# Performance work log

Hardware: AMD Instinct MI355X
Metric: run time of the kernel (lower is better)

The kernel has to match this reference:

```python
import jax, jax.numpy as jnp
import numpy as np


def _lin(x, w, b):
    # torch Linear: y = x @ w.T + b, w shape [out, in]
    return x @ w.T + b


def setup_inputs() -> dict:
    key = jax.random.key(0)
    ks = jax.random.split(key, 24)
    D, L1, L2, L3, C = 784, 128, 64, 32, 10
    B = 65536
    s = 0.05
    inp = {
        'x': jax.random.normal(ks[0], (B, D), jnp.float32),
        'W1_w': jax.random.normal(ks[1], (L1, D), jnp.float32) * s,
        'W1_b': jnp.zeros((L1,), jnp.float32),
        'U1_w': jax.random.normal(ks[2], (L1, L1), jnp.float32) * s,
        'U1_b': jnp.zeros((L1,), jnp.float32),
        'W2_w': jax.random.normal(ks[3], (L2, L1), jnp.float32) * s,
        'W2_b': jnp.zeros((L2,), jnp.float32),
        'U2_w': jax.random.normal(ks[4], (L2, L2), jnp.float32) * s,
        'U2_b': jnp.zeros((L2,), jnp.float32),
        'W3_w': jax.random.normal(ks[5], (L3, L2), jnp.float32) * s,
        'W3_b': jnp.zeros((L3,), jnp.float32),
        'U3_w': jax.random.normal(ks[6], (L3, L3), jnp.float32) * s,
        'U3_b': jnp.zeros((L3,), jnp.float32),
        'fb3_w': jax.random.normal(ks[7], (L2, L3), jnp.float32) * s,
        'fb3_b': jnp.zeros((L2,), jnp.float32),
        'fb2_w': jax.random.normal(ks[8], (L1, L2), jnp.float32) * s,
        'fb2_b': jnp.zeros((L1,), jnp.float32),
        'fb1_w': jax.random.normal(ks[9], (D, L1), jnp.float32) * s,
        'fb1_b': jnp.zeros((D,), jnp.float32),
        'clf_w': jax.random.normal(ks[10], (C, L3), jnp.float32) * s,
        'clf_b': jnp.zeros((C,), jnp.float32),
        'steps': 5,
    }
    return inp


def reference(x, W1_w, W1_b, U1_w, U1_b, W2_w, W2_b, U2_w, U2_b,
              W3_w, W3_b, U3_w, U3_b, fb3_w, fb3_b, fb2_w, fb2_b,
              fb1_w, fb1_b, clf_w, clf_b, steps):
    B = x.shape[0]
    x = x.reshape(B, -1)
    h1 = jnp.zeros((B, W1_w.shape[0]), x.dtype)
    h2 = jnp.zeros((B, W2_w.shape[0]), x.dtype)
    h3 = jnp.zeros((B, W3_w.shape[0]), x.dtype)
    for _ in range(steps):  # fixed small step count (5)
        err_h2 = h2 - _lin(h3, fb3_w, fb3_b)
        err_h1 = h1 - _lin(h2, fb2_w, fb2_b)
        err_x = x - _lin(h1, fb1_w, fb1_b)
        h3 = h3 + jnp.tanh(_lin(err_h2, W3_w, W3_b)) + jnp.tanh(_lin(h3, U3_w, U3_b))
        h2 = h2 + jnp.tanh(_lin(err_h1, W2_w, W2_b)) + jnp.tanh(_lin(h2, U2_w, U2_b))
        h1 = h1 + jnp.tanh(_lin(err_x, W1_w, W1_b)) + jnp.tanh(_lin(h1, U1_w, U1_b))
    return _lin(h3, clf_w, clf_b)
```

## Files before the change

kernel.cpp:

```cpp
#include <hip/hip_runtime.h>
#include <stdint.h>

typedef __attribute__((ext_vector_type(8))) __bf16 bf16x8;
typedef __attribute__((ext_vector_type(8))) unsigned short u16x8;
typedef __attribute__((ext_vector_type(4))) float f32x4;

#define WSF_M1 0
#define WSF_M2 16384
#define WSF_M3 20480
#define WSF_C  21504
#define F_W1T 0
#define F_M1N 102400
#define F_U1T 118784
#define F_W2T 135168
#define F_M2N 143360
#define F_U2T 147456
#define F_W3T 151552
#define F_M3N 153600
#define F_U3T 154624
#define F_CLF 155648

__device__ __forceinline__ unsigned short f2bf(float f) {
  uint32_t u = __builtin_bit_cast(uint32_t, f);
  u += 0x7fffu + ((u >> 16) & 1u);
  return (unsigned short)(u >> 16);
}

extern "C" __device__ float __ocml_native_exp2_f32(float);
__device__ __forceinline__ float tanh_fast(float x) {
  float e = __ocml_native_exp2_f32(x * 2.8853900817779268f);
  return 1.0f - 2.0f * __builtin_amdgcn_rcpf(e + 1.0f);
}

__device__ __forceinline__ f32x4 mfma16(bf16x8 a, bf16x8 b, f32x4 c) {
  return __builtin_amdgcn_mfma_f32_16x16x32_bf16(a, b, c, 0, 0, 0);
}

__device__ __forceinline__ bf16x8 lds_frag(const unsigned short* p) {
  u16x8 v = *(const u16x8*)p;
  return __builtin_bit_cast(bf16x8, v);
}
__device__ __forceinline__ bf16x8 glb_frag(const unsigned short* __restrict__ base,
                                           int fi, int lane) {
  u16x8 v = *(const u16x8*)(base + (((size_t)fi * 64 + lane) << 3));
  return __builtin_bit_cast(bf16x8, v);
}

__global__ void pcnet_prep(
    const float* __restrict__ W1_w, const float* __restrict__ W1_b,
    const float* __restrict__ W2_w, const float* __restrict__ W2_b,
    const float* __restrict__ W3_w, const float* __restrict__ W3_b,
    const float* __restrict__ fb1_w, const float* __restrict__ fb1_b,
    const float* __restrict__ fb2_w, const float* __restrict__ fb2_b,
    const float* __restrict__ fb3_w, const float* __restrict__ fb3_b,
    float* __restrict__ wsf)
{
  const int b = threadIdx.x;
  const int blk = blockIdx.x;
  if (blk < 128) {
    const int a = blk;
    float s = 0.f;
    for (int d = 0; d < 784; ++d) s += fb1_w[d*128 + a] * W1_w[b*784 + d];
    wsf[WSF_M1 + a*128 + b] = -s;
  } else if (blk < 192) {
    const int a = blk - 128;
    if (b < 64) {
      float s = 0.f;
      for (int d = 0; d < 128; ++d) s += fb2_w[d*64 + a] * W2_w[b*128 + d];
      wsf[WSF_M2 + a*64 + b] = -s;
    }
  } else if (blk < 224) {
    const int a = blk - 192;
    if (b < 32) {
      float s = 0.f;
      for (int d = 0; d < 64; ++d) s += fb3_w[d*32 + a] * W3_w[b*64 + d];
      wsf[WSF_M3 + a*32 + b] = -s;
    }
  } else if (blk == 224) {
    float s = 0.f;
    for (int d = 0; d < 784; ++d) s += fb1_b[d] * W1_w[b*784 + d];
    wsf[WSF_C + b] = W1_b[b] - s;
  } else if (blk == 225) {
    if (b < 64) {
      float s = 0.f;
      for (int d = 0; d < 128; ++d) s += fb2_b[d] * W2_w[b*128 + d];
      wsf[WSF_C + 128 + b] = W2_b[b] - s;
    }
  } else {
    if (b < 32) {
      float s = 0.f;
      for (int d = 0; d < 64; ++d) s += fb3_b[d] * W3_w[b*64 + d];
      wsf[WSF_C + 192 + b] = W3_b[b] - s;
    }
  }
}

__device__ __forceinline__ void swz_T(const float* __restrict__ src, int ld, int Kv, int Nv,
                                      int NT, unsigned short* __restrict__ dst, int f, int lane) {
  const int kt = f / NT, nt = f - kt*NT;
  const int m = lane & 15, q = lane >> 4;
  const int n = nt*16 + m;
  u16x8 v;
#pragma unroll
  for (int j = 0; j < 8; ++j) {
    const int k = kt*32 + q*8 + j;
    float val = (k < Kv && n < Nv) ? src[(size_t)n*ld + k] : 0.f;
    v[j] = f2bf(val);
  }
  *(u16x8*)(dst + (((size_t)f*64 + lane) << 3)) = v;
}
__device__ __forceinline__ void swz_R(const float* __restrict__ src, int N, int NT,
                                      unsigned short* __restrict__ dst, int f, int lane) {
  const int kt = f / NT, nt = f - kt*NT;
  const int m = lane & 15, q = lane >> 4;
  const int n = nt*16 + m;
  u16x8 v;
#pragma unroll
  for (int j = 0; j < 8; ++j) {
    const int k = kt*32 + q*8 + j;
    v[j] = f2bf(src[k*N + n]);
  }
  *(u16x8*)(dst + (((size_t)f*64 + lane) << 3)) = v;
}

__global__ void pcnet_swz(
    const float* __restrict__ W1_w, const float* __restrict__ U1_w,
    const float* __restrict__ W2_w, const float* __restrict__ U2_w,
    const float* __restrict__ W3_w, const float* __restrict__ U3_w,
    const float* __restrict__ clf_w, const float* __restrict__ wsf,
    unsigned short* __restrict__ frags)
{
  const int t = blockIdx.x*256 + threadIdx.x;
  if (t >= 305*64) return;
  const int fg = t >> 6, lane = t & 63;
  if      (fg < 200) swz_T(W1_w, 784, 784, 128, 8, frags + F_W1T, fg,       lane);
  else if (fg < 232) swz_R(wsf + WSF_M1, 128, 8,  frags + F_M1N, fg - 200, lane);
  else if (fg < 264) swz_T(U1_w, 128, 128, 128, 8, frags + F_U1T, fg - 232, lane);
  else if (fg < 280) swz_T(W2_w, 128, 128, 64, 4, frags + F_W2T, fg - 264, lane);
  else if (fg < 288) swz_R(wsf + WSF_M2, 64, 4,   frags + F_M2N, fg - 280, lane);
  else if (fg < 296) swz_T(U2_w, 64, 64, 64, 4,   frags + F_U2T, fg - 288, lane);
  else if (fg < 300) swz_T(W3_w, 64, 64, 32, 2,   frags + F_W3T, fg - 296, lane);
  else if (fg < 302) swz_R(wsf + WSF_M3, 32, 2,   frags + F_M3N, fg - 300, lane);
  else if (fg < 304) swz_T(U3_w, 32, 32, 32, 2,   frags + F_U3T, fg - 302, lane);
  else               swz_T(clf_w, 32, 32, 10, 1,  frags + F_CLF, fg - 304, lane);
}

__global__ __launch_bounds__(256, 2)
void pcnet_main(
    const float* __restrict__ x,
    const float* __restrict__ cvec,
    const float* __restrict__ U1_b, const float* __restrict__ U2_b,
    const float* __restrict__ U3_b, const float* __restrict__ clf_b,
    const unsigned short* __restrict__ frags,
    const int* __restrict__ steps_p,
    float* __restrict__ out)
{
  const int tid  = threadIdx.x;
  const int wave = tid >> 6;
  const int lane = tid & 63;
  const int q = lane >> 4;
  const int m = lane & 15;
  const int rowBase = blockIdx.x << 6;

  __shared__ unsigned short h1b[64*136];
  __shared__ unsigned short h2b[64*72];
  __shared__ unsigned short h3b[64*40];
  __shared__ unsigned short xst[2][64*40];

  const unsigned short* fW1T = frags + F_W1T;
  const unsigned short* fM1N = frags + F_M1N;
  const unsigned short* fU1T = frags + F_U1T;
  const unsigned short* fW2T = frags + F_W2T;
  const unsigned short* fM2N = frags + F_M2N;
  const unsigned short* fU2T = frags + F_U2T;
  const unsigned short* fW3T = frags + F_W3T;
  const unsigned short* fM3N = frags + F_M3N;
  const unsigned short* fU3T = frags + F_U3T;
  const unsigned short* fCLF = frags + F_CLF;

  f32x4 A1[4][2];
#pragma unroll
  for (int nt = 0; nt < 2; ++nt) {
    const float cv = cvec[(2*wave + nt)*16 + m];
    const f32x4 v = {cv, cv, cv, cv};
    A1[0][nt] = v; A1[1][nt] = v; A1[2][nt] = v; A1[3][nt] = v;
  }

  const int srow = tid >> 2;
  const int kq = (tid & 3) << 3;
  const float* __restrict__ xrow = x + (size_t)(rowBase + srow)*784;

  {
    f32x4 va = *(const f32x4*)(xrow + kq);
    f32x4 vb = *(const f32x4*)(xrow + kq + 4);
    u16x8 pk;
    pk[0]=f2bf(va[0]); pk[1]=f2bf(va[1]); pk[2]=f2bf(va[2]); pk[3]=f2bf(va[3]);
    pk[4]=f2bf(vb[0]); pk[5]=f2bf(vb[1]); pk[6]=f2bf(vb[2]); pk[7]=f2bf(vb[3]);
    *(u16x8*)(xst[0] + srow*40 + kq) = pk;
  }

  for (int kt = 0; kt < 25; ++kt) {
    __syncthreads();
    if (kt < 24) {
      const int gk = (kt + 1)*32 + kq;
      f32x4 va = {0.f,0.f,0.f,0.f}, vb = {0.f,0.f,0.f,0.f};
      if (gk < 784) { va = *(const f32x4*)(xrow + gk); vb = *(const f32x4*)(xrow + gk + 4); }
      u16x8 pk;
      pk[0]=f2bf(va[0]); pk[1]=f2bf(va[1]); pk[2]=f2bf(va[2]); pk[3]=f2bf(va[3]);
      pk[4]=f2bf(vb[0]); pk[5]=f2bf(vb[1]); pk[6]=f2bf(vb[2]); pk[7]=f2bf(vb[3]);
      *(u16x8*)(xst[(kt+1)&1] + srow*40 + kq) = pk;
    }
    const unsigned short* xb = xst[kt & 1];
    const bf16x8 a0 = lds_frag(xb + (0*16 + m)*40 + q*8);
    const bf16x8 a1 = lds_frag(xb + (1*16 + m)*40 + q*8);
    const bf16x8 a2 = lds_frag(xb + (2*16 + m)*40 + q*8);
    const bf16x8 a3 = lds_frag(xb + (3*16 + m)*40 + q*8);
#pragma unroll
    for (int nt = 0; nt < 2; ++nt) {
      const bf16x8 b = glb_frag(fW1T, kt*8 + 2*wave + nt, lane);
      A1[0][nt] = mfma16(a0, b, A1[0][nt]);
      A1[1][nt] = mfma16(a1, b, A1[1][nt]);
      A1[2][nt] = mfma16(a2, b, A1[2][nt]);
      A1[3][nt] = mfma16(a3, b, A1[3][nt]);
    }
  }

  {
    uint32_t* p = (uint32_t*)h1b;
    for (int i = tid; i < 4352; i += 256) p[i] = 0u;
    p = (uint32_t*)h2b;
    for (int i = tid; i < 2304; i += 256) p[i] = 0u;
    p = (uint32_t*)h3b;
    for (int i = tid; i < 1280; i += 256) p[i] = 0u;
  }
  f32x4 h1v[4][2], h2v[4], h3v[2];
  {
    const f32x4 z = {0.f,0.f,0.f,0.f};
#pragma unroll
    for (int rt = 0; rt < 4; ++rt) { h1v[rt][0] = z; h1v[rt][1] = z; h2v[rt] = z; }
    h3v[0] = z; h3v[1] = z;
  }

  const int nt3 = wave >> 1;
  const int rt3 = (wave & 1) << 1;
  const float c3v  = cvec[192 + nt3*16 + m];
  const float b3v  = U3_b[nt3*16 + m];
  const float c2v  = cvec[128 + wave*16 + m];
  const float b2v  = U2_b[wave*16 + m];
  const float b1v0 = U1_b[(2*wave + 0)*16 + m];
  const float b1v1 = U1_b[(2*wave + 1)*16 + m];

  __syncthreads();

  const int S = *steps_p;
  for (int s = 0; s < S; ++s) {
    bf16x8 h2f[2][4];
#pragma unroll
    for (int kt = 0; kt < 2; ++kt)
#pragma unroll
      for (int rt = 0; rt < 4; ++rt)
        h2f[kt][rt] = lds_frag(h2b + (rt*16 + m)*72 + kt*32 + q*8);
    const bf16x8 h3f0 = lds_frag(h3b + ((rt3+0)*16 + m)*40 + q*8);
    const bf16x8 h3f1 = lds_frag(h3b + ((rt3+1)*16 + m)*40 + q*8);
    bf16x8 h2s0[2], h2s1[2];
#pragma unroll
    for (int kt = 0; kt < 2; ++kt) {
      h2s0[kt] = (wave & 1) ? h2f[kt][2] : h2f[kt][0];
      h2s1[kt] = (wave & 1) ? h2f[kt][3] : h2f[kt][1];
    }

    f32x4 z3a0 = {c3v,c3v,c3v,c3v}, z3a1 = z3a0;
    f32x4 z3b0 = {b3v,b3v,b3v,b3v}, z3b1 = z3b0;
#pragma unroll
    for (int kt = 0; kt < 2; ++kt) {
      const bf16x8 b = glb_frag(fW3T, kt*2 + nt3, lane);
      z3a0 = mfma16(h2s0[kt], b, z3a0);
      z3a1 = mfma16(h2s1[kt], b, z3a1);
    }
    { const bf16x8 b = glb_frag(fM3N, nt3, lane);
      z3a0 = mfma16(h3f0, b, z3a0); z3a1 = mfma16(h3f1, b, z3a1); }
    { const bf16x8 b = glb_frag(fU3T, nt3, lane);
      z3b0 = mfma16(h3f0, b, z3b0); z3b1 = mfma16(h3f1, b, z3b1); }
#pragma unroll
    for (int r = 0; r < 4; ++r) {
      h3v[0][r] += tanh_fast(z3a0[r]) + tanh_fast(z3b0[r]);
      h3v[1][r] += tanh_fast(z3a1[r]) + tanh_fast(z3b1[r]);
    }

    f32x4 z2b[4];
    { const f32x4 v = {b2v,b2v,b2v,b2v}; z2b[0]=v; z2b[1]=v; z2b[2]=v; z2b[3]=v; }
#pragma unroll
    for (int kt = 0; kt < 2; ++kt) {
      const bf16x8 b = glb_frag(fU2T, kt*4 + wave, lane);
#pragma unroll
      for (int rt = 0; rt < 4; ++rt) z2b[rt] = mfma16(h2f[kt][rt], b, z2b[rt]);
    }
#pragma unroll
    for (int rt = 0; rt < 4; ++rt)
#pragma unroll
      for (int r = 0; r < 4; ++r) h2v[rt][r] += tanh_fast(z2b[rt][r]);

    f32x4 z2a[4];
    { const f32x4 v = {c2v,c2v,c2v,c2v}; z2a[0]=v; z2a[1]=v; z2a[2]=v; z2a[3]=v; }
#pragma unroll
    for (int kt = 0; kt < 2; ++kt) {
      const bf16x8 b = glb_frag(fM2N, kt*4 + wave, lane);
#pragma unroll
      for (int rt = 0; rt < 4; ++rt) z2a[rt] = mfma16(h2f[kt][rt], b, z2a[rt]);
    }

    f32x4 z1a[4][2], z1b[4][2];
    { const f32x4 v0 = {b1v0,b1v0,b1v0,b1v0};
      const f32x4 v1 = {b1v1,b1v1,b1v1,b1v1};
#pragma unroll
      for (int rt = 0; rt < 4; ++rt) {
        z1a[rt][0] = A1[rt][0]; z1a[rt][1] = A1[rt][1];
        z1b[rt][0] = v0;        z1b[rt][1] = v1;
      }
    }
#pragma unroll
    for (int kt = 0; kt < 4; ++kt) {
      const bf16x8 a0 = lds_frag(h1b + (0*16 + m)*136 + kt*32 + q*8);
      const bf16x8 a1 = lds_frag(h1b + (1*16 + m)*136 + kt*32 + q*8);
      const bf16x8 a2 = lds_frag(h1b + (2*16 + m)*136 + kt*32 + q*8);
      const bf16x8 a3 = lds_frag(h1b + (3*16 + m)*136 + kt*32 + q*8);
      const bf16x8 bW = glb_frag(fW2T, kt*4 + wave, lane);
      z2a[0] = mfma16(a0, bW, z2a[0]);
      z2a[1] = mfma16(a1, bW, z2a[1]);
      z2a[2] = mfma16(a2, bW, z2a[2]);
      z2a[3] = mfma16(a3, bW, z2a[3]);
      const bf16x8 bM0 = glb_frag(fM1N, kt*8 + 2*wave + 0, lane);
      const bf16x8 bM1 = glb_frag(fM1N, kt*8 + 2*wave + 1, lane);
      z1a[0][0] = mfma16(a0, bM0, z1a[0][0]); z1a[0][1] = mfma16(a0, bM1, z1a[0][1]);
      z1a[1][0] = mfma16(a1, bM0, z1a[1][0]); z1a[1][1] = mfma16(a1, bM1, z1a[1][1]);
      z1a[2][0] = mfma16(a2, bM0, z1a[2][0]); z1a[2][1] = mfma16(a2, bM1, z1a[2][1]);
      z1a[3][0] = mfma16(a3, bM0, z1a[3][0]); z1a[3][1] = mfma16(a3, bM1, z1a[3][1]);
      const bf16x8 bU0 = glb_frag(fU1T, kt*8 + 2*wave + 0, lane);
      const bf16x8 bU1 = glb_frag(fU1T, kt*8 + 2*wave + 1, lane);
      z1b[0][0] = mfma16(a0, bU0, z1b[0][0]); z1b[0][1] = mfma16(a0, bU1, z1b[0][1]);
      z1b[1][0] = mfma16(a1, bU0, z1b[1][0]); z1b[1][1] = mfma16(a1, bU1, z1b[1][1]);
      z1b[2][0] = mfma16(a2, bU0, z1b[2][0]); z1b[2][1] = mfma16(a2, bU1, z1b[2][1]);
      z1b[3][0] = mfma16(a3, bU0, z1b[3][0]); z1b[3][1] = mfma16(a3, bU1, z1b[3][1]);
    }
#pragma unroll
    for (int rt = 0; rt < 4; ++rt)
#pragma unroll
      for (int r = 0; r < 4; ++r) h2v[rt][r] += tanh_fast(z2a[rt][r]);
#pragma unroll
    for (int rt = 0; rt < 4; ++rt)
#pragma unroll
      for (int nt = 0; nt < 2; ++nt)
#pragma unroll
        for (int r = 0; r < 4; ++r)
          h1v[rt][nt][r] += tanh_fast(z1a[rt][nt][r]) + tanh_fast(z1b[rt][nt][r]);

    __syncthreads();
#pragma unroll
    for (int rt = 0; rt < 4; ++rt) {
#pragma unroll
      for (int nt = 0; nt < 2; ++nt)
#pragma unroll
        for (int r = 0; r < 4; ++r)
          h1b[(rt*16 + q*4 + r)*136 + (2*wave + nt)*16 + m] = f2bf(h1v[rt][nt][r]);
#pragma unroll
      for (int r = 0; r < 4; ++r)
        h2b[(rt*16 + q*4 + r)*72 + wave*16 + m] = f2bf(h2v[rt][r]);
    }
#pragma unroll
    for (int i = 0; i < 2; ++i)
#pragma unroll
      for (int r = 0; r < 4; ++r)
        h3b[((rt3 + i)*16 + q*4 + r)*40 + nt3*16 + m] = f2bf(h3v[i][r]);
    __syncthreads();
  }

  f32x4 o;
  { const float cb = (m < 10) ? clf_b[m] : 0.f; o = (f32x4){cb, cb, cb, cb}; }
  {
    const bf16x8 a = lds_frag(h3b + (wave*16 + m)*40 + q*8);
    const bf16x8 b = glb_frag(fCLF, 0, lane);
    o = mfma16(a, b, o);
  }
  if (m < 10) {
#pragma unroll
    for (int r = 0; r < 4; ++r) {
      const int row = rowBase + wave*16 + q*4 + r;
      out[(size_t)row*10 + m] = o[r];
    }
  }
}

extern "C" void kernel_launch(void* const* d_in, const int* in_sizes, int n_in,
                              void* d_out, int out_size, void* d_ws, size_t ws_size,
                              hipStream_t stream)
{
  (void)in_sizes; (void)n_in; (void)out_size; (void)ws_size;
  const float* x     = (const float*)d_in[0];
  const float* W1_w  = (const float*)d_in[1];
  const float* W1_b  = (const float*)d_in[2];
  const float* U1_w  = (const float*)d_in[3];
  const float* U1_b  = (const float*)d_in[4];
  const float* W2_w  = (const float*)d_in[5];
  const float* W2_b  = (const float*)d_in[6];
  const float* U2_w  = (const float*)d_in[7];
  const float* U2_b  = (const float*)d_in[8];
  const float* W3_w  = (const float*)d_in[9];
  const float* W3_b  = (const float*)d_in[10];
  const float* U3_w  = (const float*)d_in[11];
  const float* U3_b  = (const float*)d_in[12];
  const float* fb3_w = (const float*)d_in[13];
  const float* fb3_b = (const float*)d_in[14];
  const float* fb2_w = (const float*)d_in[15];
  const float* fb2_b = (const float*)d_in[16];
  const float* fb1_w = (const float*)d_in[17];
  const float* fb1_b = (const float*)d_in[18];
  const float* clf_w = (const float*)d_in[19];
  const float* clf_b = (const float*)d_in[20];
  const int*   steps = (const int*)d_in[21];

  float* wsf = (float*)d_ws;
  unsigned short* frags = (unsigned short*)d_ws + 43520;

  hipLaunchKernelGGL(pcnet_prep, dim3(227), dim3(128), 0, stream,
                     W1_w, W1_b, W2_w, W2_b, W3_w, W3_b,
                     fb1_w, fb1_b, fb2_w, fb2_b, fb3_w, fb3_b, wsf);
  hipLaunchKernelGGL(pcnet_swz, dim3(77), dim3(256), 0, stream,
                     W1_w, U1_w, W2_w, U2_w, W3_w, U3_w, clf_w, wsf, frags);
  hipLaunchKernelGGL(pcnet_main, dim3(1024), dim3(256), 0, stream,
                     x, wsf + WSF_C, U1_b, U2_b, U3_b, clf_b, frags, steps,
                     (float*)d_out);
}
```

Baseline: 545.6 us.

## Halve main-kernel row tile to 32 and parallelize prep dot products per wave

The prep kernel is rewritten so each 64-lane wave computes one output dot product with strided loads and a shuffle reduction, instead of one thread looping serially over up to 784 elements. This targets the long serial latency of the old 227-block launch. The main kernel processes 32 rows per block instead of 64, which doubles the grid to 2048 blocks and halves per-block LDS and accumulator registers to allow more occupancy. The cost is that each block re-reads the swizzled weight fragments for half as many rows, and the final classifier uses only two of the four waves.

After: 480.5 us. -11.9%, faster.

```diff
diff --git a/kernel.cpp b/kernel.cpp
--- a/kernel.cpp
+++ b/kernel.cpp
@@ -3,6 +3,7 @@
 
 typedef __attribute__((ext_vector_type(8))) __bf16 bf16x8;
 typedef __attribute__((ext_vector_type(8))) unsigned short u16x8;
+typedef __attribute__((ext_vector_type(4))) unsigned short u16x4;
 typedef __attribute__((ext_vector_type(4))) float f32x4;
 
 #define WSF_M1 0
@@ -46,7 +47,8 @@
   return __builtin_bit_cast(bf16x8, v);
 }
 
-__global__ void pcnet_prep(
+__global__ __launch_bounds__(256)
+void pcnet_prep(
     const float* __restrict__ W1_w, const float* __restrict__ W1_b,
     const float* __restrict__ W2_w, const float* __restrict__ W2_b,
     const float* __restrict__ W3_w, const float* __restrict__ W3_b,
@@ -55,43 +57,37 @@
     const float* __restrict__ fb3_w, const float* __restrict__ fb3_b,
     float* __restrict__ wsf)
 {
-  const int b = threadIdx.x;
-  const int blk = blockIdx.x;
-  if (blk < 128) {
-    const int a = blk;
-    float s = 0.f;
-    for (int d = 0; d < 784; ++d) s += fb1_w[d*128 + a] * W1_w[b*784 + d];
-    wsf[WSF_M1 + a*128 + b] = -s;
-  } else if (blk < 192) {
-    const int a = blk - 128;
-    if (b < 64) {
-      float s = 0.f;
-      for (int d = 0; d < 128; ++d) s += fb2_w[d*64 + a] * W2_w[b*128 + d];
-      wsf[WSF_M2 + a*64 + b] = -s;
-    }
-  } else if (blk < 224) {
-    const int a = blk - 192;
-    if (b < 32) {
-      float s = 0.f;
-      for (int d = 0; d < 64; ++d) s += fb3_w[d*32 + a] * W3_w[b*64 + d];
-      wsf[WSF_M3 + a*32 + b] = -s;
-    }
-  } else if (blk == 224) {
-    float s = 0.f;
-    for (int d = 0; d < 784; ++d) s += fb1_b[d] * W1_w[b*784 + d];
-    wsf[WSF_C + b] = W1_b[b] - s;
-  } else if (blk == 225) {
-    if (b < 64) {
-      float s = 0.f;
-      for (int d = 0; d < 128; ++d) s += fb2_b[d] * W2_w[b*128 + d];
-      wsf[WSF_C + 128 + b] = W2_b[b] - s;
-    }
-  } else {
-    if (b < 32) {
-      float s = 0.f;
-      for (int d = 0; d < 64; ++d) s += fb3_b[d] * W3_w[b*64 + d];
-      wsf[WSF_C + 192 + b] = W3_b[b] - s;
-    }
+  const int w    = blockIdx.x * 4 + (threadIdx.x >> 6);
+  const int lane = threadIdx.x & 63;
+  float s = 0.f;
+  if (w < 16384) {
+    const int a = w >> 7, b = w & 127;
+    for (int d = lane; d < 784; d += 64) s += fb1_w[d*128 + a] * W1_w[b*784 + d];
+  } else if (w < 20480) {
+    const int t = w - 16384, a = t >> 6, b = t & 63;
+    for (int d = lane; d < 128; d += 64) s += fb2_w[d*64 + a] * W2_w[b*128 + d];
+  } else if (w < 21504) {
+    const int t = w - 20480, a = t >> 5, b = t & 31;
+    s = fb3_w[lane*32 + a] * W3_w[b*64 + lane];
+  } else if (w < 21632) {
+    const int b = w - 21504;
+    for (int d = lane; d < 784; d += 64) s += fb1_b[d] * W1_w[b*784 + d];
+  } else if (w < 21696) {
+    const int b = w - 21632;
+    for (int d = lane; d < 128; d += 64) s += fb2_b[d] * W2_w[b*128 + d];
+  } else if (w < 21728) {
+    const int b = w - 21696;
+    s = fb3_b[lane] * W3_w[b*64 + lane];
+  }
+#pragma unroll
+  for (int off = 32; off >= 1; off >>= 1) s += __shfl_down(s, off, 64);
+  if (lane == 0) {
+    if (w < 16384)      wsf[WSF_M1 + (w >> 7)*128 + (w & 127)] = -s;
+    else if (w < 20480) { const int t = w - 16384; wsf[WSF_M2 + (t >> 6)*64 + (t & 63)] = -s; }
+    else if (w < 21504) { const int t = w - 20480; wsf[WSF_M3 + (t >> 5)*32 + (t & 31)] = -s; }
+    else if (w < 21632) { const int b = w - 21504; wsf[WSF_C + b]       = W1_b[b] - s; }
+    else if (w < 21696) { const int b = w - 21632; wsf[WSF_C + 128 + b] = W2_b[b] - s; }
+    else if (w < 21728) { const int b = w - 21696; wsf[WSF_C + 192 + b] = W3_b[b] - s; }
   }
 }
 
@@ -160,12 +156,12 @@
   const int lane = tid & 63;
   const int q = lane >> 4;
   const int m = lane & 15;
-  const int rowBase = blockIdx.x << 6;
-
-  __shared__ unsigned short h1b[64*136];
-  __shared__ unsigned short h2b[64*72];
-  __shared__ unsigned short h3b[64*40];
-  __shared__ unsigned short xst[2][64*40];
+  const int rowBase = blockIdx.x << 5;
+
+  __shared__ unsigned short h1b[32*136];
+  __shared__ unsigned short h2b[32*72];
+  __shared__ unsigned short h3b[32*40];
+  __shared__ unsigned short xst[2][32*40];
 
   const unsigned short* fW1T = frags + F_W1T;
   const unsigned short* fM1N = frags + F_M1N;
@@ -178,71 +174,64 @@
   const unsigned short* fU3T = frags + F_U3T;
   const unsigned short* fCLF = frags + F_CLF;
 
-  f32x4 A1[4][2];
+  f32x4 A1[2][2];
 #pragma unroll
   for (int nt = 0; nt < 2; ++nt) {
     const float cv = cvec[(2*wave + nt)*16 + m];
     const f32x4 v = {cv, cv, cv, cv};
-    A1[0][nt] = v; A1[1][nt] = v; A1[2][nt] = v; A1[3][nt] = v;
-  }
-
-  const int srow = tid >> 2;
-  const int kq = (tid & 3) << 3;
+    A1[0][nt] = v; A1[1][nt] = v;
+  }
+
+  const int srow = tid >> 3;
+  const int kq   = (tid & 7) << 2;
   const float* __restrict__ xrow = x + (size_t)(rowBase + srow)*784;
 
   {
     f32x4 va = *(const f32x4*)(xrow + kq);
-    f32x4 vb = *(const f32x4*)(xrow + kq + 4);
-    u16x8 pk;
+    u16x4 pk;
     pk[0]=f2bf(va[0]); pk[1]=f2bf(va[1]); pk[2]=f2bf(va[2]); pk[3]=f2bf(va[3]);
-    pk[4]=f2bf(vb[0]); pk[5]=f2bf(vb[1]); pk[6]=f2bf(vb[2]); pk[7]=f2bf(vb[3]);
-    *(u16x8*)(xst[0] + srow*40 + kq) = pk;
+    *(u16x4*)(xst[0] + srow*40 + kq) = pk;
   }
 
   for (int kt = 0; kt < 25; ++kt) {
     __syncthreads();
     if (kt < 24) {
       const int gk = (kt + 1)*32 + kq;
-      f32x4 va = {0.f,0.f,0.f,0.f}, vb = {0.f,0.f,0.f,0.f};
-      if (gk < 784) { va = *(const f32x4*)(xrow + gk); vb = *(const f32x4*)(xrow + gk + 4); }
-      u16x8 pk;
+      f32x4 va = {0.f,0.f,0.f,0.f};
+      if (gk < 784) va = *(const f32x4*)(xrow + gk);
+      u16x4 pk;
       pk[0]=f2bf(va[0]); pk[1]=f2bf(va[1]); pk[2]=f2bf(va[2]); pk[3]=f2bf(va[3]);
-      pk[4]=f2bf(vb[0]); pk[5]=f2bf(vb[1]); pk[6]=f2bf(vb[2]); pk[7]=f2bf(vb[3]);
-      *(u16x8*)(xst[(kt+1)&1] + srow*40 + kq) = pk;
+      *(u16x4*)(xst[(kt+1)&1] + srow*40 + kq) = pk;
     }
     const unsigned short* xb = xst[kt & 1];
     const bf16x8 a0 = lds_frag(xb + (0*16 + m)*40 + q*8);
     const bf16x8 a1 = lds_frag(xb + (1*16 + m)*40 + q*8);
-    const bf16x8 a2 = lds_frag(xb + (2*16 + m)*40 + q*8);
-    const bf16x8 a3 = lds_frag(xb + (3*16 + m)*40 + q*8);
 #pragma unroll
     for (int nt = 0; nt < 2; ++nt) {
       const bf16x8 b = glb_frag(fW1T, kt*8 + 2*wave + nt, lane);
       A1[0][nt] = mfma16(a0, b, A1[0][nt]);
       A1[1][nt] = mfma16(a1, b, A1[1][nt]);
-      A1[2][nt] = mfma16(a2, b, A1[2][nt]);
-      A1[3][nt] = mfma16(a3, b, A1[3][nt]);
     }
   }
 
   {
     uint32_t* p = (uint32_t*)h1b;
-    for (int i = tid; i < 4352; i += 256) p[i] = 0u;
+    for (int i = tid; i < 2176; i += 256) p[i] = 0u;
     p = (uint32_t*)h2b;
-    for (int i = tid; i < 2304; i += 256) p[i] = 0u;
+    for (int i = tid; i < 1152; i += 256) p[i] = 0u;
     p = (uint32_t*)h3b;
-    for (int i = tid; i < 1280; i += 256) p[i] = 0u;
-  }
-  f32x4 h1v[4][2], h2v[4], h3v[2];
+    for (int i = tid; i < 640; i += 256) p[i] = 0u;
+  }
+  f32x4 h1v[2][2], h2v[2], h3v;
   {
     const f32x4 z = {0.f,0.f,0.f,0.f};
 #pragma unroll
-    for (int rt = 0; rt < 4; ++rt) { h1v[rt][0] = z; h1v[rt][1] = z; h2v[rt] = z; }
-    h3v[0] = z; h3v[1] = z;
+    for (int rt = 0; rt < 2; ++rt) { h1v[rt][0] = z; h1v[rt][1] = z; h2v[rt] = z; }
+    h3v = z;
   }
 
   const int nt3 = wave >> 1;
-  const int rt3 = (wave & 1) << 1;
+  const int rt3 = wave & 1;
   const float c3v  = cvec[192 + nt3*16 + m];
   const float b3v  = U3_b[nt3*16 + m];
   const float c2v  = cvec[128 + wave*16 + m];
@@ -254,66 +243,57 @@
 
   const int S = *steps_p;
   for (int s = 0; s < S; ++s) {
-    bf16x8 h2f[2][4];
+    bf16x8 h2f[2][2];
 #pragma unroll
     for (int kt = 0; kt < 2; ++kt)
 #pragma unroll
-      for (int rt = 0; rt < 4; ++rt)
+      for (int rt = 0; rt < 2; ++rt)
         h2f[kt][rt] = lds_frag(h2b + (rt*16 + m)*72 + kt*32 + q*8);
-    const bf16x8 h3f0 = lds_frag(h3b + ((rt3+0)*16 + m)*40 + q*8);
-    const bf16x8 h3f1 = lds_frag(h3b + ((rt3+1)*16 + m)*40 + q*8);
-    bf16x8 h2s0[2], h2s1[2];
-#pragma unroll
-    for (int kt = 0; kt < 2; ++kt) {
-      h2s0[kt] = (wave & 1) ? h2f[kt][2] : h2f[kt][0];
-      h2s1[kt] = (wave & 1) ? h2f[kt][3] : h2f[kt][1];
-    }
-
-    f32x4 z3a0 = {c3v,c3v,c3v,c3v}, z3a1 = z3a0;
-    f32x4 z3b0 = {b3v,b3v,b3v,b3v}, z3b1 = z3b0;
+    const bf16x8 h3f = lds_frag(h3b + (rt3*16 + m)*40 + q*8);
+    bf16x8 h2s[2];
+#pragma unroll
+    for (int kt = 0; kt < 2; ++kt) h2s[kt] = (wave & 1) ? h2f[kt][1] : h2f[kt][0];
+
+    f32x4 z3a = {c3v,c3v,c3v,c3v};
+    f32x4 z3b = {b3v,b3v,b3v,b3v};
 #pragma unroll
     for (int kt = 0; kt < 2; ++kt) {
       const bf16x8 b = glb_frag(fW3T, kt*2 + nt3, lane);
-      z3a0 = mfma16(h2s0[kt], b, z3a0);
-      z3a1 = mfma16(h2s1[kt], b, z3a1);
-    }
-    { const bf16x8 b = glb_frag(fM3N, nt3, lane);
-      z3a0 = mfma16(h3f0, b, z3a0); z3a1 = mfma16(h3f1, b, z3a1); }
-    { const bf16x8 b = glb_frag(fU3T, nt3, lane);
-      z3b0 = mfma16(h3f0, b, z3b0); z3b1 = mfma16(h3f1, b, z3b1); }
-#pragma unroll
-    for (int r = 0; r < 4; ++r) {
-      h3v[0][r] += tanh_fast(z3a0[r]) + tanh_fast(z3b0[r]);
-      h3v[1][r] += tanh_fast(z3a1[r]) + tanh_fast(z3b1[r]);
-    }
-
-    f32x4 z2b[4];
-    { const f32x4 v = {b2v,b2v,b2v,b2v}; z2b[0]=v; z2b[1]=v; z2b[2]=v; z2b[3]=v; }
+      z3a = mfma16(h2s[kt], b, z3a);
+    }
+    { const bf16x8 b = glb_frag(fM3N, nt3, lane); z3a = mfma16(h3f, b, z3a); }
+    { const bf16x8 b = glb_frag(fU3T, nt3, lane); z3b = mfma16(h3f, b, z3b); }
+#pragma unroll
+    for (int r = 0; r < 4; ++r)
+      h3v[r] += tanh_fast(z3a[r]) + tanh_fast(z3b[r]);
+
+    f32x4 z2b[2];
+    { const f32x4 v = {b2v,b2v,b2v,b2v}; z2b[0]=v; z2b[1]=v; }
 #pragma unroll
     for (int kt = 0; kt < 2; ++kt) {
       const bf16x8 b = glb_frag(fU2T, kt*4 + wave, lane);
 #pragma unroll
-      for (int rt = 0; rt < 4; ++rt) z2b[rt] = mfma16(h2f[kt][rt], b, z2b[rt]);
-    }
-#pragma unroll
-    for (int rt = 0; rt < 4; ++rt)
+      for (int rt = 0; rt < 2; ++rt) z2b[rt] = mfma16(h2f[kt][rt], b, z2b[rt]);
+    }
+#pragma unroll
+    for (int rt = 0; rt < 2; ++rt)
 #pragma unroll
       for (int r = 0; r < 4; ++r) h2v[rt][r] += tanh_fast(z2b[rt][r]);
 
-    f32x4 z2a[4];
-    { const f32x4 v = {c2v,c2v,c2v,c2v}; z2a[0]=v; z2a[1]=v; z2a[2]=v; z2a[3]=v; }
+    f32x4 z2a[2];
+    { const f32x4 v = {c2v,c2v,c2v,c2v}; z2a[0]=v; z2a[1]=v; }
 #pragma unroll
     for (int kt = 0; kt < 2; ++kt) {
       const bf16x8 b = glb_frag(fM2N, kt*4 + wave, lane);
 #pragma unroll
-      for (int rt = 0; rt < 4; ++rt) z2a[rt] = mfma16(h2f[kt][rt], b, z2a[rt]);
-    }
-
-    f32x4 z1a[4][2], z1b[4][2];
+      for (int rt = 0; rt < 2; ++rt) z2a[rt] = mfma16(h2f[kt][rt], b, z2a[rt]);
+    }
+
+    f32x4 z1a[2][2], z1b[2][2];
     { const f32x4 v0 = {b1v0,b1v0,b1v0,b1v0};
       const f32x4 v1 = {b1v1,b1v1,b1v1,b1v1};
 #pragma unroll
-      for (int rt = 0; rt < 4; ++rt) {
+      for (int rt = 0; rt < 2; ++rt) {
         z1a[rt][0] = A1[rt][0]; z1a[rt][1] = A1[rt][1];
         z1b[rt][0] = v0;        z1b[rt][1] = v1;
       }
@@ -322,32 +302,24 @@
     for (int kt = 0; kt < 4; ++kt) {
       const bf16x8 a0 = lds_frag(h1b + (0*16 + m)*136 + kt*32 + q*8);
       const bf16x8 a1 = lds_frag(h1b + (1*16 + m)*136 + kt*32 + q*8);
-      const bf16x8 a2 = lds_frag(h1b + (2*16 + m)*136 + kt*32 + q*8);
-      const bf16x8 a3 = lds_frag(h1b + (3*16 + m)*136 + kt*32 + q*8);
       const bf16x8 bW = glb_frag(fW2T, kt*4 + wave, lane);
       z2a[0] = mfma16(a0, bW, z2a[0]);
       z2a[1] = mfma16(a1, bW, z2a[1]);
-      z2a[2] = mfma16(a2, bW, z2a[2]);
-      z2a[3] = mfma16(a3, bW, z2a[3]);
       const bf16x8 bM0 = glb_frag(fM1N, kt*8 + 2*wave + 0, lane);
       const bf16x8 bM1 = glb_frag(fM1N, kt*8 + 2*wave + 1, lane);
       z1a[0][0] = mfma16(a0, bM0, z1a[0][0]); z1a[0][1] = mfma16(a0, bM1, z1a[0][1]);
       z1a[1][0] = mfma16(a1, bM0, z1a[1][0]); z1a[1][1] = mfma16(a1, bM1, z1a[1][1]);
-      z1a[2][0] = mfma16(a2, bM0, z1a[2][0]); z1a[2][1] = mfma16(a2, bM1, z1a[2][1]);
-      z1a[3][0] = mfma16(a3, bM0, z1a[3][0]); z1a[3][1] = mfma16(a3, bM1, z1a[3][1]);
       const bf16x8 bU0 = glb_frag(fU1T, kt*8 + 2*wave + 0, lane);
       const bf16x8 bU1 = glb_frag(fU1T, kt*8 + 2*wave + 1, lane);
       z1b[0][0] = mfma16(a0, bU0, z1b[0][0]); z1b[0][1] = mfma16(a0, bU1, z1b[0][1]);
       z1b[1][0] = mfma16(a1, bU0, z1b[1][0]); z1b[1][1] = mfma16(a1, bU1, z1b[1][1]);
-      z1b[2][0] = mfma16(a2, bU0, z1b[2][0]); z1b[2][1] = mfma16(a2, bU1, z1b[2][1]);
-      z1b[3][0] = mfma16(a3, bU0, z1b[3][0]); z1b[3][1] = mfma16(a3, bU1, z1b[3][1]);
-    }
-#pragma unroll
-    for (int rt = 0; rt < 4; ++rt)
+    }
+#pragma unroll
+    for (int rt = 0; rt < 2; ++rt)
 #pragma unroll
       for (int r = 0; r < 4; ++r) h2v[rt][r] += tanh_fast(z2a[rt][r]);
 #pragma unroll
-    for (int rt = 0; rt < 4; ++rt)
+    for (int rt = 0; rt < 2; ++rt)
 #pragma unroll
       for (int nt = 0; nt < 2; ++nt)
 #pragma unroll
@@ -356,7 +328,7 @@
 
     __syncthreads();
 #pragma unroll
-    for (int rt = 0; rt < 4; ++rt) {
+    for (int rt = 0; rt < 2; ++rt) {
 #pragma unroll
       for (int nt = 0; nt < 2; ++nt)
 #pragma unroll
@@ -367,25 +339,23 @@
         h2b[(rt*16 + q*4 + r)*72 + wave*16 + m] = f2bf(h2v[rt][r]);
     }
 #pragma unroll
-    for (int i = 0; i < 2; ++i)
-#pragma unroll
-      for (int r = 0; r < 4; ++r)
-        h3b[((rt3 + i)*16 + q*4 + r)*40 + nt3*16 + m] = f2bf(h3v[i][r]);
+    for (int r = 0; r < 4; ++r)
+      h3b[(rt3*16 + q*4 + r)*40 + nt3*16 + m] = f2bf(h3v[r]);
     __syncthreads();
   }
 
-  f32x4 o;
-  { const float cb = (m < 10) ? clf_b[m] : 0.f; o = (f32x4){cb, cb, cb, cb}; }
-  {
+  if (wave < 2) {
+    f32x4 o;
+    { const float cb = (m < 10) ? clf_b[m] : 0.f; o = (f32x4){cb, cb, cb, cb}; }
     const bf16x8 a = lds_frag(h3b + (wave*16 + m)*40 + q*8);
     const bf16x8 b = glb_frag(fCLF, 0, lane);
     o = mfma16(a, b, o);
-  }
-  if (m < 10) {
-#pragma unroll
-    for (int r = 0; r < 4; ++r) {
-      const int row = rowBase + wave*16 + q*4 + r;
-      out[(size_t)row*10 + m] = o[r];
+    if (m < 10) {
+#pragma unroll
+      for (int r = 0; r < 4; ++r) {
+        const int row = rowBase + wave*16 + q*4 + r;
+        out[(size_t)row*10 + m] = o[r];
+      }
     }
   }
 }
@@ -421,12 +391,12 @@
   float* wsf = (float*)d_ws;
   unsigned short* frags = (unsigned short*)d_ws + 43520;
 
-  hipLaunchKernelGGL(pcnet_prep, dim3(227), dim3(128), 0, stream,
+  hipLaunchKernelGGL(pcnet_prep, dim3(5432), dim3(256), 0, stream,
                      W1_w, W1_b, W2_w, W2_b, W3_w, W3_b,
                      fb1_w, fb1_b, fb2_w, fb2_b, fb3_w, fb3_b, wsf);
   hipLaunchKernelGGL(pcnet_swz, dim3(77), dim3(256), 0, stream,
                      W1_w, U1_w, W2_w, U2_w, W3_w, U3_w, clf_w, wsf, frags);
-  hipLaunchKernelGGL(pcnet_main, dim3(1024), dim3(256), 0, stream,
+  hipLaunchKernelGGL(pcnet_main, dim3(2048), dim3(256), 0, stream,
                      x, wsf + WSF_C, U1_b, U2_b, U3_b, clf_b, frags, steps,
                      (float*)d_out);
 }
```
